# Kernel optimization log

Measured on AMD Instinct MI355X. Metric: run time of the kernel, lower is better.

The kernel has to match this reference:

```python
import jax, jax.numpy as jnp
import numpy as np

N, E = 50000, 800000
IN_C, HID, HEADS, OUT_C = 128, 64, 4, 64
NEG_SLOPE = 0.2


def _gat_layer(x, src, dst, W, a_src, a_dst, b, heads, out_dim, concat):
    n = x.shape[0]
    h = (x @ W).reshape(n, heads, out_dim)                      # [N,H,D]
    s_src = jnp.einsum('nhd,hd->nh', h, a_src)                  # [N,H]
    s_dst = jnp.einsum('nhd,hd->nh', h, a_dst)
    e = jax.nn.leaky_relu(s_src[src] + s_dst[dst], NEG_SLOPE)   # [Etot,H]
    m = jax.ops.segment_max(e, dst, num_segments=n)             # per-dst max (self-loops => no empty segments)
    w = jnp.exp(e - m[dst])
    denom = jax.ops.segment_sum(w, dst, num_segments=n)
    alpha = w / denom[dst]                                      # segment softmax over incoming edges
    msg = h[src] * alpha[..., None]                             # [Etot,H,D] edge gather + weight
    out = jax.ops.segment_sum(msg, dst, num_segments=n)         # scatter-sum aggregate
    out = out.reshape(n, heads * out_dim) if concat else out.mean(axis=1)
    return out + b


def setup_inputs() -> dict:
    key = jax.random.key(0)
    ks = jax.random.split(key, 10)
    x = jax.random.normal(ks[0], (N, IN_C), dtype=jnp.float32)
    edge_index = jax.random.randint(ks[1], (2, E), 0, N, dtype=jnp.int64)
    s1 = 1.0 / np.sqrt(IN_C)
    s2 = 1.0 / np.sqrt(HID * HEADS)
    return {
        'x': x,
        'edge_index': edge_index,
        'W1': jax.random.normal(ks[2], (IN_C, HEADS * HID), dtype=jnp.float32) * s1,
        'a_src1': jax.random.normal(ks[3], (HEADS, HID), dtype=jnp.float32) * s1,
        'a_dst1': jax.random.normal(ks[4], (HEADS, HID), dtype=jnp.float32) * s1,
        'b1': jnp.zeros((HEADS * HID,), dtype=jnp.float32),
        'W2': jax.random.normal(ks[5], (HEADS * HID, OUT_C), dtype=jnp.float32) * s2,
        'a_src2': jax.random.normal(ks[6], (1, OUT_C), dtype=jnp.float32) * s2,
        'a_dst2': jax.random.normal(ks[7], (1, OUT_C), dtype=jnp.float32) * s2,
        'b2': jnp.zeros((OUT_C,), dtype=jnp.float32),
    }


def reference(x, edge_index, W1, a_src1, a_dst1, b1, W2, a_src2, a_dst2, b2):
    n = x.shape[0]
    loop = jnp.arange(n, dtype=edge_index.dtype)
    src = jnp.concatenate([edge_index[0], loop])  # PyG GATConv adds self-loops
    dst = jnp.concatenate([edge_index[1], loop])
    # dropout layers are identity in eval mode
    h = _gat_layer(x, src, dst, W1, a_src1, a_dst1, b1, HEADS, HID, concat=True)
    h = jax.nn.elu(h)
    h = _gat_layer(h, src, dst, W2, a_src2, a_dst2, b2, 1, OUT_C, concat=False)
    return jnp.min(h, axis=0)
```

## Files before the change

kernel.cpp:

```cpp
#include <hip/hip_runtime.h>
#include <math.h>

typedef unsigned short ushort_t;
typedef __attribute__((ext_vector_type(8))) _Float16 f16x8;
typedef __attribute__((ext_vector_type(4))) float f32x4;


__device__ inline unsigned fenc(float f) {
    unsigned u = __float_as_uint(f);
    return (u & 0x80000000u) ? ~u : (u | 0x80000000u);
}
__device__ inline float fdec(unsigned u) {
    return __uint_as_float((u & 0x80000000u) ? (u ^ 0x80000000u) : ~u);
}

__device__ inline float wrsum(float v) {
    #pragma unroll
    for (int m = 32; m; m >>= 1) v += __shfl_xor(v, m, 64);
    return v;
}
__device__ inline float lrelu(float x) { return x > 0.f ? x : 0.2f * x; }

__device__ inline ushort_t f2h(float f) {
    _Float16 h = (_Float16)f;
    union { _Float16 h; ushort_t u; } cv;
    cv.h = h;
    return cv.u;
}

#define FMAMIX_LO(acc, pk, w) \
    asm("v_fma_mix_f32 %0, %1, %2, %0 op_sel:[0,0,0] op_sel_hi:[1,0,0]" \
        : "+v"(acc) : "v"(pk), "v"(w))
#define FMAMIX_HI(acc, pk, w) \
    asm("v_fma_mix_f32 %0, %1, %2, %0 op_sel:[1,0,0] op_sel_hi:[1,0,0]" \
        : "+v"(acc) : "v"(pk), "v"(w))

__global__ __launch_bounds__(256) void pre_kernel(const float* __restrict__ W1,
                                                  const float* __restrict__ W2,
                                                  const float* __restrict__ a_src2,
                                                  const float* __restrict__ a_dst2,
                                                  ushort_t* __restrict__ W1s,
                                                  ushort_t* __restrict__ W2s,
                                                  float* __restrict__ va,
                                                  float* __restrict__ vb,
                                                  unsigned* __restrict__ minenc,
                                                  int* __restrict__ gtot) {
    int bid = blockIdx.x;
    int tid = threadIdx.x;
    if (bid < 128) {
        int idx = bid * 256 + tid;
        int j = idx & 7;
        int lane = (idx >> 3) & 63;
        int ct = (idx >> 9) & 15;
        int kc = (idx >> 13) & 3;
        int k = kc * 32 + (lane >> 4) * 8 + j;
        int c = ct * 16 + (lane & 15);
        W1s[idx] = f2h(W1[k * 256 + c]);
    } else if (bid < 192) {
        int idx = (bid - 128) * 256 + tid;
        int j = idx & 7;
        int lane = (idx >> 3) & 63;
        int ct = (idx >> 9) & 3;
        int kc = idx >> 11;
        int k = kc * 32 + (lane >> 4) * 8 + j;
        int c = ct * 16 + (lane & 15);
        W2s[idx] = f2h(W2[k * 64 + c]);
    } else {
        int k = tid;
        float sa = 0.f, sb = 0.f;
        #pragma unroll 8
        for (int c = 0; c < 64; c++) {
            float w = W2[k * 64 + c];
            sa += w * a_src2[c];
            sb += w * a_dst2[c];
        }
        va[k] = sa;
        vb[k] = sb;
        if (tid < 64) minenc[tid] = 0xFFFFFFFFu;
        gtot[tid] = 0;
    }
}

__global__ __launch_bounds__(256) void front_kernel(const float* __restrict__ x,
                                                    const ushort_t* __restrict__ W1s,
                                                    const float* __restrict__ a_src,
                                                    const float* __restrict__ a_dst,
                                                    ushort_t* __restrict__ h1b,
                                                    float* __restrict__ ssrc,
                                                    float* __restrict__ sdst,
                                                    const int* __restrict__ ei,
                                                    int* __restrict__ bh,
                                                    int* __restrict__ gtot,
                                                    int N, int E, int Etot,
                                                    int nb16, int NBA, int BB) {
    __shared__ float ss[16 * 257];
    __shared__ float ps[256];
    int bid = blockIdx.x;
    int tid = threadIdx.x;

    if (bid >= nb16) {
        int* h = (int*)ps;
        int blk = bid - nb16;
        h[tid] = 0;
        __syncthreads();
        int i0 = blk * 4096 + tid;
        #pragma unroll
        for (int e = 0; e < 16; e++) {
            int i = i0 + e * 256;
            if (i < Etot) {
                int d = (i < E) ? ei[E + i] : (i - E);
                atomicAdd(&h[d >> 8], 1);
            }
        }
        __syncthreads();
        if (tid < BB) {
            bh[tid * NBA + blk] = h[tid];
            atomicAdd(&gtot[tid], h[tid]);
        }
        return;
    }

    int base = bid * 16;
    {
        const float4* xv = (const float4*)(x + (size_t)base * 128);
        float4* xs4 = (float4*)ss;
        #pragma unroll
        for (int i = tid; i < 512; i += 256) {
            int row = i >> 5;
            float4 v = (base + row < N) ? xv[i] : make_float4(0.f, 0.f, 0.f, 0.f);
            xs4[row * 33 + (i & 31)] = v;
        }
    }
    __syncthreads();

    int lane = tid & 63, wv = tid >> 6;
    int m = lane & 15, q = lane >> 4;
    f16x8 afrag[4];
    #pragma unroll
    for (int kc = 0; kc < 4; kc++) {
        const float* xp = ss + m * 132 + kc * 32 + q * 8;
        float4 xa = *(const float4*)xp;
        float4 xb = *(const float4*)(xp + 4);
        f16x8 af;
        af[0] = (_Float16)xa.x; af[1] = (_Float16)xa.y;
        af[2] = (_Float16)xa.z; af[3] = (_Float16)xa.w;
        af[4] = (_Float16)xb.x; af[5] = (_Float16)xb.y;
        af[6] = (_Float16)xb.z; af[7] = (_Float16)xb.w;
        afrag[kc] = af;
    }
    __syncthreads();

    #pragma unroll
    for (int t = 0; t < 4; t++) {
        int ct = wv * 4 + t;
        f32x4 acc = {0.f, 0.f, 0.f, 0.f};
        #pragma unroll
        for (int kc = 0; kc < 4; kc++) {
            f16x8 bfrag = *(const f16x8*)(W1s + (((size_t)(kc * 16 + ct) * 64 + lane) << 3));
            acc = __builtin_amdgcn_mfma_f32_16x16x32_f16(afrag[kc], bfrag, acc, 0, 0, 0);
        }
        #pragma unroll
        for (int reg = 0; reg < 4; reg++) {
            ss[(q * 4 + reg) * 257 + ct * 16 + m] = acc[reg];
        }
    }
    __syncthreads();

    int dd = tid & 63, jj = tid >> 6;
    #pragma unroll
    for (int t2 = 0; t2 < 4; t2++) {
        int j = jj + t2 * 4;
        int n = base + j;
        if (n < N) {
            const float* row = ss + j * 257 + dd * 4;
            unsigned p0 = (unsigned)f2h(row[0]) | ((unsigned)f2h(row[1]) << 16);
            unsigned p1 = (unsigned)f2h(row[2]) | ((unsigned)f2h(row[3]) << 16);
            *(uint2*)(h1b + (size_t)n * 256 + dd * 4) = make_uint2(p0, p1);
        }
    }
    int j = tid & 15, hh2 = (tid >> 4) & 3, which = (tid >> 6) & 1, half = tid >> 7;
    const float* av = which ? a_dst : a_src;
    int cbase = hh2 * 64 + half * 32;
    float sum = 0.f;
    #pragma unroll
    for (int i = 0; i < 32; i++) {
        int ii = (i + 8 * hh2) & 31;
        sum += ss[j * 257 + cbase + ii] * av[cbase + ii];
    }
    ps[tid] = sum;
    __syncthreads();
    if (half == 0) {
        float tot = sum + ps[tid + 128];
        int n = base + j;
        if (n < N) (which ? sdst : ssrc)[n * 4 + hh2] = tot;
    }
}

__global__ __launch_bounds__(256) void scan2_kernel(int* __restrict__ bh,
                                                    const int* __restrict__ gtot,
                                                    int* __restrict__ bstart,
                                                    int NBA, int BB) {
    __shared__ int sm[256];
    int b = blockIdx.x, t = threadIdx.x;
    if (b < BB) {
        int v = (t < NBA) ? bh[b * NBA + t] : 0;
        sm[t] = v;
        __syncthreads();
        for (int o = 1; o < 256; o <<= 1) {
            int a = (t >= o) ? sm[t - o] : 0;
            __syncthreads();
            sm[t] += a;
            __syncthreads();
        }
        if (t < NBA) bh[b * NBA + t] = sm[t] - v;
    } else {
        int v = (t < BB) ? gtot[t] : 0;
        sm[t] = v;
        __syncthreads();
        for (int o = 1; o < 256; o <<= 1) {
            int a = (t >= o) ? sm[t - o] : 0;
            __syncthreads();
            sm[t] += a;
            __syncthreads();
        }
        if (t < BB) bstart[t] = sm[t] - v;
        if (t == BB - 1) bstart[BB] = sm[t];
    }
}

__global__ __launch_bounds__(256) void scat_kernel(const int* __restrict__ ei,
                                                   const int* __restrict__ bh,
                                                   const int* __restrict__ bstart,
                                                   int* __restrict__ srcbuf,
                                                   int E, int Etot, int NBA, int BB) {
    __shared__ int h[256];
    __shared__ int loff[256];
    __shared__ int gb[256];
    __shared__ int su[4096];
    __shared__ int sp[4096];
    int t = threadIdx.x, blk = blockIdx.x;
    h[t] = 0;
    __syncthreads();
    int i0 = blk * 4096;
    int blkcnt = min(4096, Etot - i0);

    int rb[16];
    #pragma unroll
    for (int e = 0; e < 16; e++) {
        int i = i0 + e * 256 + t;
        rb[e] = -1;
        if (i < Etot) {
            int d = (i < E) ? ei[E + i] : (i - E);
            int b = d >> 8;
            int r = atomicAdd(&h[b], 1);
            rb[e] = (b << 12) | r;
        }
    }
    __syncthreads();

    loff[t] = h[t];
    gb[t] = (t < BB) ? (bstart[t] + bh[t * NBA + blk]) : 0;
    __syncthreads();
    for (int o = 1; o < 256; o <<= 1) {
        int a = (t >= o) ? loff[t - o] : 0;
        __syncthreads();
        loff[t] += a;
        __syncthreads();
    }

    #pragma unroll
    for (int e = 0; e < 16; e++) {
        int i = i0 + e * 256 + t;
        if (i < Etot) {
            int s = (i < E) ? ei[i] : (i - E);
            int d = (i < E) ? ei[E + i] : (i - E);
            int b = rb[e] >> 12;
            int r = rb[e] & 0xFFF;
            int slot = loff[b] - h[b] + r;
            su[slot] = s | ((d & 255) << 16);
            sp[slot] = gb[b] + r;
        }
    }
    __syncthreads();

    for (int k = t; k < blkcnt; k += 256) {
        srcbuf[sp[k]] = su[k];
    }
}

__global__ __launch_bounds__(256) void csr_kernel(const int* __restrict__ bstart,
                                                  int* __restrict__ srcbuf,
                                                  int* __restrict__ rowptr, int N) {
    __shared__ int eb[8192];
    __shared__ unsigned short rr[8192];
    __shared__ int h[256];
    __shared__ int off[256];
    int b = blockIdx.x, t = threadIdx.x;
    int s0 = bstart[b];
    int cnt = bstart[b + 1] - s0;
    if (cnt > 8192) cnt = 8192;
    h[t] = 0;
    __syncthreads();
    for (int j = t; j < cnt; j += 256) {
        int u = srcbuf[s0 + j];
        eb[j] = u;
        rr[j] = (unsigned short)atomicAdd(&h[u >> 16], 1);
    }
    __syncthreads();
    off[t] = h[t];
    __syncthreads();
    for (int o = 1; o < 256; o <<= 1) {
        int a = (t >= o) ? off[t - o] : 0;
        __syncthreads();
        off[t] += a;
        __syncthreads();
    }
    int excl = off[t] - h[t];
    int d = b * 256 + t;
    if (d <= N) rowptr[d] = s0 + excl;
    __syncthreads();
    h[t] = excl;
    __syncthreads();
    for (int j = t; j < cnt; j += 256) {
        int u = eb[j];
        srcbuf[s0 + h[u >> 16] + rr[j]] = u & 0xFFFF;
    }
}

__global__ __launch_bounds__(256) void agg1_kernel(const int* __restrict__ rowptr,
                                                   const int* __restrict__ srcbuf,
                                                   const float* __restrict__ ssrc,
                                                   const float* __restrict__ sdst,
                                                   const ushort_t* __restrict__ h1b,
                                                   const float* __restrict__ b1,
                                                   const float* __restrict__ va,
                                                   const float* __restrict__ vb,
                                                   ushort_t* __restrict__ x2b,
                                                   float* __restrict__ ssrc2,
                                                   float* __restrict__ sdst2, int N) {
    __shared__ int    s_sh[4][64];
    __shared__ float4 w_sh[4][64];
    int lane = threadIdx.x & 63, w = threadIdx.x >> 6;
    int li = lane & 31, half = lane >> 5;
    int hh = li >> 3;
    int d = blockIdx.x * 4 + w;
    if (d >= N) return;
    int row = rowptr[d], end = rowptr[d + 1];
    float4 sd = *(const float4*)(sdst + d * 4);
    float lx = 0.f, ly = 0.f, lz = 0.f, lw = 0.f;
    float a0 = 0.f, a1 = 0.f, a2 = 0.f, a3 = 0.f;
    float a4 = 0.f, a5 = 0.f, a6 = 0.f, a7 = 0.f;

    for (int base = row; base < end; base += 64) {
        int cnt = min(64, end - base);
        bool valid = lane < cnt;
        int s = valid ? srcbuf[base + lane] : 0;
        float4 ssv = *(const float4*)(ssrc + s * 4);
        float w0 = valid ? __expf(lrelu(ssv.x + sd.x)) : 0.f;
        float w1 = valid ? __expf(lrelu(ssv.y + sd.y)) : 0.f;
        float w2 = valid ? __expf(lrelu(ssv.z + sd.z)) : 0.f;
        float w3 = valid ? __expf(lrelu(ssv.w + sd.w)) : 0.f;
        lx += w0; ly += w1; lz += w2; lw += w3;
        s_sh[w][lane] = s;
        w_sh[w][lane] = make_float4(w0, w1, w2, w3);
        int cnt8 = (cnt + 7) & ~7;
        for (int j = 0; j < cnt8; j += 8) {
            int ea = j + half, eb = j + 2 + half, ec = j + 4 + half, ed = j + 6 + half;
            int sa_ = s_sh[w][ea], sb_ = s_sh[w][eb], sc_ = s_sh[w][ec], sd_ = s_sh[w][ed];
            float wa = ((const float*)(w_sh[w] + ea))[hh];
            float wb = ((const float*)(w_sh[w] + eb))[hh];
            float wc = ((const float*)(w_sh[w] + ec))[hh];
            float wd = ((const float*)(w_sh[w] + ed))[hh];
            uint4 ua = *(const uint4*)(h1b + (size_t)sa_ * 256 + li * 8);
            uint4 ub = *(const uint4*)(h1b + (size_t)sb_ * 256 + li * 8);
            uint4 uc = *(const uint4*)(h1b + (size_t)sc_ * 256 + li * 8);
            uint4 ud = *(const uint4*)(h1b + (size_t)sd_ * 256 + li * 8);
            FMAMIX_LO(a0, ua.x, wa); FMAMIX_HI(a1, ua.x, wa);
            FMAMIX_LO(a2, ua.y, wa); FMAMIX_HI(a3, ua.y, wa);
            FMAMIX_LO(a4, ua.z, wa); FMAMIX_HI(a5, ua.z, wa);
            FMAMIX_LO(a6, ua.w, wa); FMAMIX_HI(a7, ua.w, wa);
            FMAMIX_LO(a0, ub.x, wb); FMAMIX_HI(a1, ub.x, wb);
            FMAMIX_LO(a2, ub.y, wb); FMAMIX_HI(a3, ub.y, wb);
            FMAMIX_LO(a4, ub.z, wb); FMAMIX_HI(a5, ub.z, wb);
            FMAMIX_LO(a6, ub.w, wb); FMAMIX_HI(a7, ub.w, wb);
            FMAMIX_LO(a0, uc.x, wc); FMAMIX_HI(a1, uc.x, wc);
            FMAMIX_LO(a2, uc.y, wc); FMAMIX_HI(a3, uc.y, wc);
            FMAMIX_LO(a4, uc.z, wc); FMAMIX_HI(a5, uc.z, wc);
            FMAMIX_LO(a6, uc.w, wc); FMAMIX_HI(a7, uc.w, wc);
            FMAMIX_LO(a0, ud.x, wd); FMAMIX_HI(a1, ud.x, wd);
            FMAMIX_LO(a2, ud.y, wd); FMAMIX_HI(a3, ud.y, wd);
            FMAMIX_LO(a4, ud.z, wd); FMAMIX_HI(a5, ud.z, wd);
            FMAMIX_LO(a6, ud.w, wd); FMAMIX_HI(a7, ud.w, wd);
        }
    }
    a0 += __shfl_xor(a0, 32, 64); a1 += __shfl_xor(a1, 32, 64);
    a2 += __shfl_xor(a2, 32, 64); a3 += __shfl_xor(a3, 32, 64);
    a4 += __shfl_xor(a4, 32, 64); a5 += __shfl_xor(a5, 32, 64);
    a6 += __shfl_xor(a6, 32, 64); a7 += __shfl_xor(a7, 32, 64);
    float l0 = wrsum(lx), l1 = wrsum(ly), l2 = wrsum(lz), l3 = wrsum(lw);
    float lh = hh == 0 ? l0 : hh == 1 ? l1 : hh == 2 ? l2 : l3;
    float rl = 1.f / lh;
    int c8 = li * 8;
    float4 b1a = *(const float4*)(b1 + c8);
    float4 b1b = *(const float4*)(b1 + c8 + 4);
    float v0 = a0 * rl + b1a.x, v1 = a1 * rl + b1a.y;
    float v2 = a2 * rl + b1a.z, v3 = a3 * rl + b1a.w;
    float v4 = a4 * rl + b1b.x, v5 = a5 * rl + b1b.y;
    float v6 = a6 * rl + b1b.z, v7 = a7 * rl + b1b.w;
    v0 = v0 > 0.f ? v0 : __expf(v0) - 1.f;
    v1 = v1 > 0.f ? v1 : __expf(v1) - 1.f;
    v2 = v2 > 0.f ? v2 : __expf(v2) - 1.f;
    v3 = v3 > 0.f ? v3 : __expf(v3) - 1.f;
    v4 = v4 > 0.f ? v4 : __expf(v4) - 1.f;
    v5 = v5 > 0.f ? v5 : __expf(v5) - 1.f;
    v6 = v6 > 0.f ? v6 : __expf(v6) - 1.f;
    v7 = v7 > 0.f ? v7 : __expf(v7) - 1.f;
    if (half == 0) {
        unsigned p0 = (unsigned)f2h(v0) | ((unsigned)f2h(v1) << 16);
        unsigned p1 = (unsigned)f2h(v2) | ((unsigned)f2h(v3) << 16);
        unsigned p2 = (unsigned)f2h(v4) | ((unsigned)f2h(v5) << 16);
        unsigned p3 = (unsigned)f2h(v6) | ((unsigned)f2h(v7) << 16);
        *(uint4*)(x2b + (size_t)d * 256 + c8) = make_uint4(p0, p1, p2, p3);
    }
    float4 vaa = *(const float4*)(va + c8), vab = *(const float4*)(va + c8 + 4);
    float4 vba = *(const float4*)(vb + c8), vbb = *(const float4*)(vb + c8 + 4);
    float sa = v0 * vaa.x + v1 * vaa.y + v2 * vaa.z + v3 * vaa.w
             + v4 * vab.x + v5 * vab.y + v6 * vab.z + v7 * vab.w;
    float sb = v0 * vba.x + v1 * vba.y + v2 * vba.z + v3 * vba.w
             + v4 * vbb.x + v5 * vbb.y + v6 * vbb.z + v7 * vbb.w;
    sa = wrsum(sa) * 0.5f;
    sb = wrsum(sb) * 0.5f;
    if (lane == 0) { ssrc2[d] = sa; sdst2[d] = sb; }
}

__global__ __launch_bounds__(256) void gemmz_kernel(const ushort_t* __restrict__ x2b,
                                                    const ushort_t* __restrict__ W2s,
                                                    const float* __restrict__ b2,
                                                    ushort_t* __restrict__ zh, int N) {
    int base = blockIdx.x * 32;
    int tid = threadIdx.x;
    int lane = tid & 63, wv = tid >> 6;
    int m = lane & 15, q = lane >> 4;
    int c = wv * 16 + m;
    float bc = b2[c];

    #pragma unroll
    for (int h = 0; h < 2; h++) {
        int rbase = base + h * 16;
        bool rowok = (rbase + m) < N;
        const ushort_t* xrow = x2b + (size_t)(rbase + m) * 256;
        f32x4 acc = {0.f, 0.f, 0.f, 0.f};
        #pragma unroll
        for (int kc = 0; kc < 8; kc++) {
            f16x8 af = {0, 0, 0, 0, 0, 0, 0, 0};
            if (rowok) af = *(const f16x8*)(xrow + kc * 32 + q * 8);
            f16x8 bf = *(const f16x8*)(W2s + (((size_t)(kc * 4 + wv) * 64 + lane) << 3));
            acc = __builtin_amdgcn_mfma_f32_16x16x32_f16(af, bf, acc, 0, 0, 0);
        }
        #pragma unroll
        for (int reg = 0; reg < 4; reg++) {
            int n = rbase + q * 4 + reg;
            if (n < N) zh[(size_t)n * 64 + c] = f2h(acc[reg] + bc);
        }
    }
}

__global__ __launch_bounds__(256) void aggz_kernel(const int* __restrict__ rowptr,
                                                   const int* __restrict__ srcbuf,
                                                   const float* __restrict__ ssrc,
                                                   const float* __restrict__ sdst,
                                                   const ushort_t* __restrict__ zh,
                                                   unsigned* __restrict__ minenc, int N) {
    __shared__ int   s_sh[4][64];
    __shared__ float w_sh[4][64];
    __shared__ float smc[4][64];
    int lane = threadIdx.x & 63, w = threadIdx.x >> 6;
    int k = lane & 7, g = lane >> 3;
    float m0 = INFINITY, m1 = INFINITY, m2 = INFINITY, m3 = INFINITY;
    float m4 = INFINITY, m5 = INFINITY, m6 = INFINITY, m7 = INFINITY;

    for (int d0 = blockIdx.x * 4; d0 < N; d0 += gridDim.x * 4) {
        int d = d0 + w;
        if (d < N) {
            int row = rowptr[d], end = rowptr[d + 1];
            float sdv = sdst[d];
            float lacc = 0.f;
            float a0 = 0.f, a1 = 0.f, a2 = 0.f, a3 = 0.f;
            float a4 = 0.f, a5 = 0.f, a6 = 0.f, a7 = 0.f;
            for (int base = row; base < end; base += 64) {
                int cnt = min(64, end - base);
                bool valid = lane < cnt;
                int s = valid ? srcbuf[base + lane] : 0;
                float wt = valid ? __expf(lrelu(ssrc[s] + sdv)) : 0.f;
                lacc += wt;
                s_sh[w][lane] = s;
                w_sh[w][lane] = wt;
                int cnt8 = (cnt + 7) & ~7;
                for (int j = 0; j < cnt8; j += 8) {
                    int e = j + g;
                    int sj = s_sh[w][e];
                    float wj = w_sh[w][e];
                    uint4 u = *(const uint4*)(zh + (size_t)sj * 64 + k * 8);
                    FMAMIX_LO(a0, u.x, wj); FMAMIX_HI(a1, u.x, wj);
                    FMAMIX_LO(a2, u.y, wj); FMAMIX_HI(a3, u.y, wj);
                    FMAMIX_LO(a4, u.z, wj); FMAMIX_HI(a5, u.z, wj);
                    FMAMIX_LO(a6, u.w, wj); FMAMIX_HI(a7, u.w, wj);
                }
            }
            #define GRED(a) { a += __shfl_xor(a, 8, 64); a += __shfl_xor(a, 16, 64); a += __shfl_xor(a, 32, 64); }
            GRED(a0) GRED(a1) GRED(a2) GRED(a3)
            GRED(a4) GRED(a5) GRED(a6) GRED(a7)
            #undef GRED
            float rl = 1.f / wrsum(lacc);
            m0 = fminf(m0, a0 * rl); m1 = fminf(m1, a1 * rl);
            m2 = fminf(m2, a2 * rl); m3 = fminf(m3, a3 * rl);
            m4 = fminf(m4, a4 * rl); m5 = fminf(m5, a5 * rl);
            m6 = fminf(m6, a6 * rl); m7 = fminf(m7, a7 * rl);
        }
    }
    if (g == 0) {
        float* sp = &smc[w][k * 8];
        sp[0] = m0; sp[1] = m1; sp[2] = m2; sp[3] = m3;
        sp[4] = m4; sp[5] = m5; sp[6] = m6; sp[7] = m7;
    }
    __syncthreads();
    if (w == 0) {
        float v = fminf(fminf(smc[0][lane], smc[1][lane]),
                        fminf(smc[2][lane], smc[3][lane]));
        atomicMin(&minenc[lane], fenc(v));
    }
}

__global__ void decode_kernel(const unsigned* __restrict__ minenc, float* __restrict__ out) {
    int d = threadIdx.x;
    if (d < 64) out[d] = fdec(minenc[d]);
}

extern "C" void kernel_launch(void* const* d_in, const int* in_sizes, int n_in,
                              void* d_out, int out_size, void* d_ws, size_t ws_size,
                              hipStream_t stream) {
    const float* x      = (const float*)d_in[0];
    const int*   ei     = (const int*)d_in[1];
    const float* W1     = (const float*)d_in[2];
    const float* a_src1 = (const float*)d_in[3];
    const float* a_dst1 = (const float*)d_in[4];
    const float* b1     = (const float*)d_in[5];
    const float* W2     = (const float*)d_in[6];
    const float* a_src2 = (const float*)d_in[7];
    const float* a_dst2 = (const float*)d_in[8];
    const float* b2     = (const float*)d_in[9];
    float* out = (float*)d_out;

    const int N = in_sizes[0] / 128;
    const int E = in_sizes[1] / 2;
    const int Etot = E + N;
    const int Epad = Etot + 64;
    const int M = N + 1;

    const int BB  = ((N - 1) >> 8) + 1;
    const int NBA = (Etot + 4095) / 4096;

    float* ws = (float*)d_ws;
    ushort_t* h1b = (ushort_t*)ws;
    ushort_t* x2b = (ushort_t*)(ws + (size_t)N * 128);
    ushort_t* zh  = (ushort_t*)(ws + (size_t)N * 256);
    ushort_t* W1s = (ushort_t*)(ws + (size_t)N * 320);
    ushort_t* W2s = (ushort_t*)(ws + (size_t)N * 320 + 16384);
    float* ssrc1  = ws + (size_t)N * 320 + 24576;
    float* sdst1  = ssrc1 + (size_t)N * 4;
    float* ssrc2  = sdst1 + (size_t)N * 4;
    float* sdst2  = ssrc2 + N;
    float* va     = sdst2 + N;
    float* vb     = va + 256;
    int*   bh     = (int*)(vb + 256);
    int*   rowptr = bh + M;
    int*   gtot   = rowptr + M;
    int*   bstart = gtot + 256;
    int*   srcbuf = bstart + 256;
    unsigned* minenc = (unsigned*)(srcbuf + Epad);

    int nb16 = (N + 15) / 16;
    int nb32 = (N + 31) / 32;
    int nb4 = (N + 3) / 4;
    int nbz = 2048;

    pre_kernel<<<193, 256, 0, stream>>>(W1, W2, a_src2, a_dst2, W1s, W2s, va, vb,
                                        minenc, gtot);
    front_kernel<<<nb16 + NBA, 256, 0, stream>>>(x, W1s, a_src1, a_dst1, h1b, ssrc1, sdst1,
                                                 ei, bh, gtot, N, E, Etot, nb16, NBA, BB);
    scan2_kernel<<<BB + 1, 256, 0, stream>>>(bh, gtot, bstart, NBA, BB);
    scat_kernel<<<NBA, 256, 0, stream>>>(ei, bh, bstart, srcbuf, E, Etot, NBA, BB);
    csr_kernel<<<BB, 256, 0, stream>>>(bstart, srcbuf, rowptr, N);

    agg1_kernel<<<nb4, 256, 0, stream>>>(rowptr, srcbuf, ssrc1, sdst1, h1b, b1,
                                         va, vb, x2b, ssrc2, sdst2, N);
    gemmz_kernel<<<nb32, 256, 0, stream>>>(x2b, W2s, b2, zh, N);
    aggz_kernel<<<nbz, 256, 0, stream>>>(rowptr, srcbuf, ssrc2, sdst2, zh, minenc, N);
    decode_kernel<<<1, 64, 0, stream>>>(minenc, out);
}
```

Measured before the change: 269.4 us.

## Slice layer-1 features into channel slabs and aggregate each slab separately

The layer-1 feature matrix is stored as 8 separate 32-channel slabs instead of 256-channel rows. Aggregation runs one block per (destination group, slab), so each block's random gathers touch a 3.2 MB slab that fits in cache. Partial attention scores for layer 2 are written per slab and summed inside the GEMM kernel. The cost is 8x more blocks, softmax weights recomputed per slab (each head twice), and extra partial-score traffic.

Result: slower. 392.3 us (+45.6%).

```diff
diff --git a/kernel.cpp b/kernel.cpp
--- a/kernel.cpp
+++ b/kernel.cpp
@@ -175,7 +175,8 @@
             const float* row = ss + j * 257 + dd * 4;
             unsigned p0 = (unsigned)f2h(row[0]) | ((unsigned)f2h(row[1]) << 16);
             unsigned p1 = (unsigned)f2h(row[2]) | ((unsigned)f2h(row[3]) << 16);
-            *(uint2*)(h1b + (size_t)n * 256 + dd * 4) = make_uint2(p0, p1);
+            *(uint2*)(h1b + (size_t)(dd >> 3) * N * 32 + (size_t)n * 32 + (dd & 7) * 4)
+                = make_uint2(p0, p1);
         }
     }
     int j = tid & 15, hh2 = (tid >> 4) & 3, which = (tid >> 6) & 1, half = tid >> 7;
@@ -327,27 +328,31 @@
     }
 }
 
-__global__ __launch_bounds__(256) void agg1_kernel(const int* __restrict__ rowptr,
-                                                   const int* __restrict__ srcbuf,
-                                                   const float* __restrict__ ssrc,
-                                                   const float* __restrict__ sdst,
-                                                   const ushort_t* __restrict__ h1b,
-                                                   const float* __restrict__ b1,
-                                                   const float* __restrict__ va,
-                                                   const float* __restrict__ vb,
-                                                   ushort_t* __restrict__ x2b,
-                                                   float* __restrict__ ssrc2,
-                                                   float* __restrict__ sdst2, int N) {
-    __shared__ int    s_sh[4][64];
-    __shared__ float4 w_sh[4][64];
+__global__ __launch_bounds__(256) void aggslice_kernel(const int* __restrict__ rowptr,
+                                                       const int* __restrict__ srcbuf,
+                                                       const float* __restrict__ ssrc,
+                                                       const float* __restrict__ sdst,
+                                                       const ushort_t* __restrict__ h1b,
+                                                       const float* __restrict__ b1,
+                                                       const float* __restrict__ va,
+                                                       const float* __restrict__ vb,
+                                                       ushort_t* __restrict__ x2b,
+                                                       float* __restrict__ sapart,
+                                                       float* __restrict__ sbpart, int N) {
+    __shared__ int   s_sh[4][64];
+    __shared__ float w_sh[4][64];
+    int bid = blockIdx.x;
+    int k = bid & 7;
+    int grp = bid >> 3;
     int lane = threadIdx.x & 63, w = threadIdx.x >> 6;
-    int li = lane & 31, half = lane >> 5;
-    int hh = li >> 3;
-    int d = blockIdx.x * 4 + w;
+    int d = grp * 4 + w;
     if (d >= N) return;
+    int h = k >> 1;
+    int k4 = lane & 3, g = lane >> 2;
     int row = rowptr[d], end = rowptr[d + 1];
-    float4 sd = *(const float4*)(sdst + d * 4);
-    float lx = 0.f, ly = 0.f, lz = 0.f, lw = 0.f;
+    float sdv = sdst[d * 4 + h];
+    const ushort_t* hsl = h1b + (size_t)k * N * 32;
+    float lacc = 0.f;
     float a0 = 0.f, a1 = 0.f, a2 = 0.f, a3 = 0.f;
     float a4 = 0.f, a5 = 0.f, a6 = 0.f, a7 = 0.f;
 
@@ -355,54 +360,31 @@
         int cnt = min(64, end - base);
         bool valid = lane < cnt;
         int s = valid ? srcbuf[base + lane] : 0;
-        float4 ssv = *(const float4*)(ssrc + s * 4);
-        float w0 = valid ? __expf(lrelu(ssv.x + sd.x)) : 0.f;
-        float w1 = valid ? __expf(lrelu(ssv.y + sd.y)) : 0.f;
-        float w2 = valid ? __expf(lrelu(ssv.z + sd.z)) : 0.f;
-        float w3 = valid ? __expf(lrelu(ssv.w + sd.w)) : 0.f;
-        lx += w0; ly += w1; lz += w2; lw += w3;
+        float wv = valid ? __expf(lrelu(ssrc[s * 4 + h] + sdv)) : 0.f;
+        lacc += wv;
         s_sh[w][lane] = s;
-        w_sh[w][lane] = make_float4(w0, w1, w2, w3);
-        int cnt8 = (cnt + 7) & ~7;
-        for (int j = 0; j < cnt8; j += 8) {
-            int ea = j + half, eb = j + 2 + half, ec = j + 4 + half, ed = j + 6 + half;
-            int sa_ = s_sh[w][ea], sb_ = s_sh[w][eb], sc_ = s_sh[w][ec], sd_ = s_sh[w][ed];
-            float wa = ((const float*)(w_sh[w] + ea))[hh];
-            float wb = ((const float*)(w_sh[w] + eb))[hh];
-            float wc = ((const float*)(w_sh[w] + ec))[hh];
-            float wd = ((const float*)(w_sh[w] + ed))[hh];
-            uint4 ua = *(const uint4*)(h1b + (size_t)sa_ * 256 + li * 8);
-            uint4 ub = *(const uint4*)(h1b + (size_t)sb_ * 256 + li * 8);
-            uint4 uc = *(const uint4*)(h1b + (size_t)sc_ * 256 + li * 8);
-            uint4 ud = *(const uint4*)(h1b + (size_t)sd_ * 256 + li * 8);
-            FMAMIX_LO(a0, ua.x, wa); FMAMIX_HI(a1, ua.x, wa);
-            FMAMIX_LO(a2, ua.y, wa); FMAMIX_HI(a3, ua.y, wa);
-            FMAMIX_LO(a4, ua.z, wa); FMAMIX_HI(a5, ua.z, wa);
-            FMAMIX_LO(a6, ua.w, wa); FMAMIX_HI(a7, ua.w, wa);
-            FMAMIX_LO(a0, ub.x, wb); FMAMIX_HI(a1, ub.x, wb);
-            FMAMIX_LO(a2, ub.y, wb); FMAMIX_HI(a3, ub.y, wb);
-            FMAMIX_LO(a4, ub.z, wb); FMAMIX_HI(a5, ub.z, wb);
-            FMAMIX_LO(a6, ub.w, wb); FMAMIX_HI(a7, ub.w, wb);
-            FMAMIX_LO(a0, uc.x, wc); FMAMIX_HI(a1, uc.x, wc);
-            FMAMIX_LO(a2, uc.y, wc); FMAMIX_HI(a3, uc.y, wc);
-            FMAMIX_LO(a4, uc.z, wc); FMAMIX_HI(a5, uc.z, wc);
-            FMAMIX_LO(a6, uc.w, wc); FMAMIX_HI(a7, uc.w, wc);
-            FMAMIX_LO(a0, ud.x, wd); FMAMIX_HI(a1, ud.x, wd);
-            FMAMIX_LO(a2, ud.y, wd); FMAMIX_HI(a3, ud.y, wd);
-            FMAMIX_LO(a4, ud.z, wd); FMAMIX_HI(a5, ud.z, wd);
-            FMAMIX_LO(a6, ud.w, wd); FMAMIX_HI(a7, ud.w, wd);
-        }
-    }
-    a0 += __shfl_xor(a0, 32, 64); a1 += __shfl_xor(a1, 32, 64);
-    a2 += __shfl_xor(a2, 32, 64); a3 += __shfl_xor(a3, 32, 64);
-    a4 += __shfl_xor(a4, 32, 64); a5 += __shfl_xor(a5, 32, 64);
-    a6 += __shfl_xor(a6, 32, 64); a7 += __shfl_xor(a7, 32, 64);
-    float l0 = wrsum(lx), l1 = wrsum(ly), l2 = wrsum(lz), l3 = wrsum(lw);
-    float lh = hh == 0 ? l0 : hh == 1 ? l1 : hh == 2 ? l2 : l3;
-    float rl = 1.f / lh;
-    int c8 = li * 8;
-    float4 b1a = *(const float4*)(b1 + c8);
-    float4 b1b = *(const float4*)(b1 + c8 + 4);
+        w_sh[w][lane] = wv;
+        int cnt16 = (cnt + 15) & ~15;
+        for (int j = 0; j < cnt16; j += 16) {
+            int e = j + g;
+            int se = s_sh[w][e];
+            float we = w_sh[w][e];
+            uint4 u = *(const uint4*)(hsl + (size_t)se * 32 + k4 * 8);
+            FMAMIX_LO(a0, u.x, we); FMAMIX_HI(a1, u.x, we);
+            FMAMIX_LO(a2, u.y, we); FMAMIX_HI(a3, u.y, we);
+            FMAMIX_LO(a4, u.z, we); FMAMIX_HI(a5, u.z, we);
+            FMAMIX_LO(a6, u.w, we); FMAMIX_HI(a7, u.w, we);
+        }
+    }
+    #define GRED(a) { a += __shfl_xor(a, 4, 64); a += __shfl_xor(a, 8, 64); \
+                      a += __shfl_xor(a, 16, 64); a += __shfl_xor(a, 32, 64); }
+    GRED(a0) GRED(a1) GRED(a2) GRED(a3)
+    GRED(a4) GRED(a5) GRED(a6) GRED(a7)
+    #undef GRED
+    float rl = 1.f / wrsum(lacc);
+    int c = k * 32 + k4 * 8;
+    float4 b1a = *(const float4*)(b1 + c);
+    float4 b1b = *(const float4*)(b1 + c + 4);
     float v0 = a0 * rl + b1a.x, v1 = a1 * rl + b1a.y;
     float v2 = a2 * rl + b1a.z, v3 = a3 * rl + b1a.w;
     float v4 = a4 * rl + b1b.x, v5 = a5 * rl + b1b.y;
@@ -415,30 +397,48 @@
     v5 = v5 > 0.f ? v5 : __expf(v5) - 1.f;
     v6 = v6 > 0.f ? v6 : __expf(v6) - 1.f;
     v7 = v7 > 0.f ? v7 : __expf(v7) - 1.f;
-    if (half == 0) {
+    if (g == 0) {
         unsigned p0 = (unsigned)f2h(v0) | ((unsigned)f2h(v1) << 16);
         unsigned p1 = (unsigned)f2h(v2) | ((unsigned)f2h(v3) << 16);
         unsigned p2 = (unsigned)f2h(v4) | ((unsigned)f2h(v5) << 16);
         unsigned p3 = (unsigned)f2h(v6) | ((unsigned)f2h(v7) << 16);
-        *(uint4*)(x2b + (size_t)d * 256 + c8) = make_uint4(p0, p1, p2, p3);
-    }
-    float4 vaa = *(const float4*)(va + c8), vab = *(const float4*)(va + c8 + 4);
-    float4 vba = *(const float4*)(vb + c8), vbb = *(const float4*)(vb + c8 + 4);
+        *(uint4*)(x2b + (size_t)k * N * 32 + (size_t)d * 32 + k4 * 8)
+            = make_uint4(p0, p1, p2, p3);
+    }
+    float4 vaa = *(const float4*)(va + c), vab = *(const float4*)(va + c + 4);
+    float4 vba = *(const float4*)(vb + c), vbb = *(const float4*)(vb + c + 4);
     float sa = v0 * vaa.x + v1 * vaa.y + v2 * vaa.z + v3 * vaa.w
              + v4 * vab.x + v5 * vab.y + v6 * vab.z + v7 * vab.w;
     float sb = v0 * vba.x + v1 * vba.y + v2 * vba.z + v3 * vba.w
              + v4 * vbb.x + v5 * vbb.y + v6 * vbb.z + v7 * vbb.w;
-    sa = wrsum(sa) * 0.5f;
-    sb = wrsum(sb) * 0.5f;
-    if (lane == 0) { ssrc2[d] = sa; sdst2[d] = sb; }
+    sa += __shfl_xor(sa, 1, 64); sa += __shfl_xor(sa, 2, 64);
+    sb += __shfl_xor(sb, 1, 64); sb += __shfl_xor(sb, 2, 64);
+    if (lane == 0) { sapart[d * 8 + k] = sa; sbpart[d * 8 + k] = sb; }
 }
 
 __global__ __launch_bounds__(256) void gemmz_kernel(const ushort_t* __restrict__ x2b,
                                                     const ushort_t* __restrict__ W2s,
                                                     const float* __restrict__ b2,
+                                                    const float* __restrict__ sapart,
+                                                    const float* __restrict__ sbpart,
+                                                    float* __restrict__ ssrc2,
+                                                    float* __restrict__ sdst2,
                                                     ushort_t* __restrict__ zh, int N) {
     int base = blockIdx.x * 32;
     int tid = threadIdx.x;
+    if (tid < 32) {
+        int r = base + tid;
+        if (r < N) {
+            float sa = 0.f, sb = 0.f;
+            #pragma unroll
+            for (int k = 0; k < 8; k++) {
+                sa += sapart[r * 8 + k];
+                sb += sbpart[r * 8 + k];
+            }
+            ssrc2[r] = sa;
+            sdst2[r] = sb;
+        }
+    }
     int lane = tid & 63, wv = tid >> 6;
     int m = lane & 15, q = lane >> 4;
     int c = wv * 16 + m;
@@ -448,12 +448,12 @@
     for (int h = 0; h < 2; h++) {
         int rbase = base + h * 16;
         bool rowok = (rbase + m) < N;
-        const ushort_t* xrow = x2b + (size_t)(rbase + m) * 256;
         f32x4 acc = {0.f, 0.f, 0.f, 0.f};
         #pragma unroll
         for (int kc = 0; kc < 8; kc++) {
             f16x8 af = {0, 0, 0, 0, 0, 0, 0, 0};
-            if (rowok) af = *(const f16x8*)(xrow + kc * 32 + q * 8);
+            if (rowok) af = *(const f16x8*)(x2b + (size_t)kc * N * 32
+                                            + (size_t)(rbase + m) * 32 + q * 8);
             f16x8 bf = *(const f16x8*)(W2s + (((size_t)(kc * 4 + wv) * 64 + lane) << 3));
             acc = __builtin_amdgcn_mfma_f32_16x16x32_f16(af, bf, acc, 0, 0, 0);
         }
@@ -578,10 +578,12 @@
     int*   bstart = gtot + 256;
     int*   srcbuf = bstart + 256;
     unsigned* minenc = (unsigned*)(srcbuf + Epad);
+    float* sapart = (float*)(minenc + 64);
+    float* sbpart = sapart + (size_t)N * 8;
 
     int nb16 = (N + 15) / 16;
     int nb32 = (N + 31) / 32;
-    int nb4 = (N + 3) / 4;
+    int nbs = ((N + 3) / 4) * 8;
     int nbz = 2048;
 
     pre_kernel<<<193, 256, 0, stream>>>(W1, W2, a_src2, a_dst2, W1s, W2s, va, vb,
@@ -592,9 +594,10 @@
     scat_kernel<<<NBA, 256, 0, stream>>>(ei, bh, bstart, srcbuf, E, Etot, NBA, BB);
     csr_kernel<<<BB, 256, 0, stream>>>(bstart, srcbuf, rowptr, N);
 
-    agg1_kernel<<<nb4, 256, 0, stream>>>(rowptr, srcbuf, ssrc1, sdst1, h1b, b1,
-                                         va, vb, x2b, ssrc2, sdst2, N);
-    gemmz_kernel<<<nb32, 256, 0, stream>>>(x2b, W2s, b2, zh, N);
+    aggslice_kernel<<<nbs, 256, 0, stream>>>(rowptr, srcbuf, ssrc1, sdst1, h1b, b1,
+                                             va, vb, x2b, sapart, sbpart, N);
+    gemmz_kernel<<<nb32, 256, 0, stream>>>(x2b, W2s, b2, sapart, sbpart,
+                                           ssrc2, sdst2, zh, N);
     aggz_kernel<<<nbz, 256, 0, stream>>>(rowptr, srcbuf, ssrc2, sdst2, zh, minenc, N);
     decode_kernel<<<1, 64, 0, stream>>>(minenc, out);
 }
```
